# Kernel optimization log

Hardware: AMD Instinct MI355X
Metric: run time of the kernel (lower is better)

Reference implementation:

```python
import jax, jax.numpy as jnp
import numpy as np

B, C, H, W_IMG, P, D = 64, 3, 224, 224, 16, 768
N_PATCH = (H // P) * (W_IMG // P)  # 196
SEQ = N_PATCH + 1                  # 197


def setup_inputs() -> dict:
    key = jax.random.key(0)
    k1, k2, k3, k4, k5 = jax.random.split(key, 5)
    in_feat = P * P * C  # 768
    return {
        "x": jax.random.normal(k1, (B, C, H, W_IMG), dtype=jnp.float32),
        "W": jax.random.normal(k2, (in_feat, D), dtype=jnp.float32) * (1.0 / np.sqrt(in_feat)),
        "b": jax.random.normal(k3, (D,), dtype=jnp.float32) * 0.02,
        "pos_table": jax.random.normal(k4, (SEQ, D), dtype=jnp.float32) * 0.02,
        "class_token": jax.random.normal(k5, (1, 1, D), dtype=jnp.float32),
    }


def _patchify(x):
    # Matches torch loop: patch (i,j) is x[:, :, i*P:(i+1)*P, j*P:(j+1)*P].reshape(B, C*P*P)
    # i.e. features ordered channel-major then row then col within patch.
    b = x.shape[0]
    hp, wp = H // P, W_IMG // P
    x = x.reshape(b, C, hp, P, wp, P)              # (B,C,hp,P,wp,P)
    x = x.transpose(0, 2, 4, 1, 3, 5)              # (B,hp,wp,C,P,P)
    return x.reshape(b, hp * wp, C * P * P)        # (B,N,C*P*P)


def reference(x, W, b, pos_table, class_token):
    patches = _patchify(x)                          # (B, N, C*P*P)
    tokens = jnp.einsum("bnf,fd->bnd", patches, W) + b  # (B, N, D)
    cls = jnp.broadcast_to(class_token, (x.shape[0], 1, D))
    seq = jnp.concatenate([cls, tokens], axis=1)    # (B, SEQ, D)
    # positions = arange(SEQ) broadcast over batch -> embedding lookup
    return seq + pos_table[None, :, :]              # dropout is identity in eval
```

## Files before the change

### kernel.cpp

```cpp
#include <hip/hip_runtime.h>
#include <hip/hip_bf16.h>

namespace {

constexpr int Bsz = 64, Cch = 3, Himg = 224, Wimg = 224, Ppat = 16;
constexpr int Dm = 768, NPW = 14, NPATCH = 196, SEQn = 197;
constexpr int Mtot = Bsz * NPATCH;
constexpr int Ktot = 768, Ntot = 768;
constexpr int BM = 64, BN = 128, BK = 64;
constexpr int MT = Mtot / BM;
constexpr int NT = Ntot / BN;
constexpr int KT = Ktot / BK;
constexpr int NBLK = MT * NT;
constexpr int TAF = BM * BK;
constexpr int TB = BN * BK;
constexpr size_t WT_ELEMS = (size_t)NT * KT * TB;
constexpr size_t WS_NEED = WT_ELEMS * 2;
constexpr int WPREP_BLK = (Ktot / 8) * Ntot / 256;
constexpr int CLS_BLK = Bsz * Dm / 256;

typedef __attribute__((ext_vector_type(8))) short bf16x8;
typedef __attribute__((ext_vector_type(4))) float f32x4;

__device__ inline unsigned short f2bf(float f) {
  __bf16 h = (__bf16)f;
  union { __bf16 h; unsigned short u; } c;
  c.h = h;
  return c.u;
}

union Pack8 { unsigned short s[8]; uint4 v; };

__global__ void prep_kernel(const float* __restrict__ W,
                            const float* __restrict__ pos, const float* __restrict__ cls,
                            unsigned short* __restrict__ Wt, float* __restrict__ out) {
  const int bid = blockIdx.x;
  const int t = threadIdx.x;
  if (bid < WPREP_BLK) {
    int cid = bid * 256 + t;
    int kc = cid / Ntot;
    int n = cid - kc * Ntot;
    int nb = n >> 7;
    int np = n & 127;
    int kt = kc >> 3;
    int k8 = (kc & 7) * 8;
    Pack8 p;
#pragma unroll
    for (int j = 0; j < 8; ++j) p.s[j] = f2bf(W[(size_t)(kc * 8 + j) * Ntot + n]);
    int sidx = (np * BK + k8) ^ ((np & 7) << 3);
    *reinterpret_cast<uint4*>(Wt + (size_t)(nb * KT + kt) * TB + sidx) = p.v;
  } else {
    int i = (bid - WPREP_BLK) * 256 + t;
    int b = i / Dm;
    int d = i - b * Dm;
    out[(size_t)b * (SEQn * Dm) + d] = cls[d] + pos[d];
  }
}

__global__ __launch_bounds__(128, 2)
void gemm_kernel(const float* __restrict__ x, const unsigned short* __restrict__ Wt,
                 const float* __restrict__ bias, const float* __restrict__ pos,
                 float* __restrict__ out) {
  __shared__ float Af[TAF];
  __shared__ unsigned short B[TB];

  const int orig = blockIdx.x;
  const int wg = (orig & 7) * (NBLK / 8) + (orig >> 3);
  const int bm = wg / NT;
  const int bn = wg - bm * NT;

  const int t = threadIdx.x;
  const int lane = t & 63;
  const int wc = t >> 6;
  const int fr = lane & 15, fq = lane >> 4;

  const int klocal = (((t & 15) ^ ((t >> 4) & 7)) << 2);
  int rowbase[8];
#pragma unroll
  for (int i = 0; i < 8; ++i) {
    int r = i * 8 + (t >> 4);
    int m = bm * BM + r;
    int b = m / NPATCH;
    int pidx = m - b * NPATCH;
    int ph = pidx / NPW, pw = pidx - ph * NPW;
    rowbase[i] = ((b * Cch) * Himg + ph * Ppat) * Wimg + pw * Ppat;
  }
  const unsigned short* bSrc = Wt + (size_t)(bn * KT) * TB + t * 8;

  auto STAGE = [&](int kt) {
    int kg = kt * BK + klocal;
    int c = kg >> 8, pi = (kg >> 4) & 15, pj = kg & 15;
    int koff = (c * Himg + pi) * Wimg + pj;
#pragma unroll
    for (int i = 0; i < 8; ++i)
      __builtin_amdgcn_global_load_lds(
          (const __attribute__((address_space(1))) unsigned int*)(x + rowbase[i] + koff),
          (__attribute__((address_space(3))) unsigned int*)(&Af[t * 4 + i * 512]),
          16, 0, 0);
#pragma unroll
    for (int i = 0; i < 8; ++i)
      __builtin_amdgcn_global_load_lds(
          (const __attribute__((address_space(1))) unsigned int*)(bSrc + kt * TB + i * 1024),
          (__attribute__((address_space(3))) unsigned int*)(&B[t * 8 + i * 1024]),
          16, 0, 0);
  };

  f32x4 acc[4][4];
#pragma unroll
  for (int mi = 0; mi < 4; ++mi)
#pragma unroll
    for (int ni = 0; ni < 4; ++ni) acc[mi][ni] = {0.f, 0.f, 0.f, 0.f};

  for (int kt = 0; kt < KT; ++kt) {
    STAGE(kt);
    __syncthreads();
#pragma unroll
    for (int ks = 0; ks < 2; ++ks) {
      bf16x8 af[4], bfr[4];
#pragma unroll
      for (int mi = 0; mi < 4; ++mi) {
        int r = mi * 16 + fr;
        int g0 = ks * 8 + fq * 2;
        float4 a0 = *reinterpret_cast<const float4*>(&Af[r * 64 + ((g0 ^ (r & 7)) << 2)]);
        float4 a1 = *reinterpret_cast<const float4*>(&Af[r * 64 + (((g0 + 1) ^ (r & 7)) << 2)]);
        Pack8 p;
        p.s[0] = f2bf(a0.x); p.s[1] = f2bf(a0.y); p.s[2] = f2bf(a0.z); p.s[3] = f2bf(a0.w);
        p.s[4] = f2bf(a1.x); p.s[5] = f2bf(a1.y); p.s[6] = f2bf(a1.z); p.s[7] = f2bf(a1.w);
        af[mi] = *reinterpret_cast<const bf16x8*>(&p);
      }
#pragma unroll
      for (int ni = 0; ni < 4; ++ni) {
        int n = wc * 64 + ni * 16 + fr;
        int idx = (n * BK + ks * 32 + fq * 8) ^ ((n & 7) << 3);
        bfr[ni] = *reinterpret_cast<const bf16x8*>(&B[idx]);
      }
#pragma unroll
      for (int mi = 0; mi < 4; ++mi)
#pragma unroll
        for (int ni = 0; ni < 4; ++ni)
          acc[mi][ni] = __builtin_amdgcn_mfma_f32_16x16x32_bf16(
              af[mi], bfr[ni], acc[mi][ni], 0, 0, 0);
    }
    if (kt + 1 < KT) __syncthreads();
  }

  const int n0 = bn * BN + wc * 64;
  float bv[4];
#pragma unroll
  for (int ni = 0; ni < 4; ++ni) bv[ni] = bias[n0 + ni * 16 + fr];
#pragma unroll
  for (int mi = 0; mi < 4; ++mi) {
#pragma unroll
    for (int j = 0; j < 4; ++j) {
      int m = bm * BM + mi * 16 + fq * 4 + j;
      int b = m / NPATCH;
      int s = m - b * NPATCH + 1;
      float* orow = out + ((size_t)b * SEQn + s) * Dm + n0;
      const float* prow = pos + (size_t)s * Dm + n0;
#pragma unroll
      for (int ni = 0; ni < 4; ++ni) {
        int d = ni * 16 + fr;
        orow[d] = acc[mi][ni][j] + bv[ni] + prow[d];
      }
    }
  }
}

}

extern "C" void kernel_launch(void* const* d_in, const int* in_sizes, int n_in,
                              void* d_out, int out_size, void* d_ws, size_t ws_size,
                              hipStream_t stream) {
  const float* x = (const float*)d_in[0];
  const float* W = (const float*)d_in[1];
  const float* bias = (const float*)d_in[2];
  const float* pos = (const float*)d_in[3];
  const float* cls = (const float*)d_in[4];
  float* out = (float*)d_out;
  unsigned short* Wt = (unsigned short*)d_ws;

  prep_kernel<<<WPREP_BLK + CLS_BLK, 256, 0, stream>>>(W, pos, cls, Wt, out);
  gemm_kernel<<<NBLK, 128, 0, stream>>>(x, Wt, bias, pos, out);
}
```

Baseline: 46.31 us.

## Convert A tile to bf16 once at staging and use 4 waves per block

The activation tile is now loaded into registers with plain vector loads, converted to bf16 once, and written to a swizzled bf16 LDS buffer, instead of being copied as fp32 straight to LDS and reconverted by every wave on every fragment read. The block grows from 2 to 4 waves in a 2x2 layout, each holding half the accumulators, and the launch bounds ask for higher occupancy. This removes redundant conversions and halves A-tile LDS use. The cost is that the A load no longer goes asynchronously into LDS, so global latency sits in registers before the barrier.

New measurement: 38.74 us (median of 2 runs). -16.3%, faster.

```diff
diff --git a/kernel.cpp b/kernel.cpp
--- a/kernel.cpp
+++ b/kernel.cpp
@@ -12,10 +12,9 @@
 constexpr int NT = Ntot / BN;
 constexpr int KT = Ktot / BK;
 constexpr int NBLK = MT * NT;
-constexpr int TAF = BM * BK;
+constexpr int TA = BM * BK;
 constexpr int TB = BN * BK;
 constexpr size_t WT_ELEMS = (size_t)NT * KT * TB;
-constexpr size_t WS_NEED = WT_ELEMS * 2;
 constexpr int WPREP_BLK = (Ktot / 8) * Ntot / 256;
 constexpr int CLS_BLK = Bsz * Dm / 256;
 
@@ -57,11 +56,11 @@
   }
 }
 
-__global__ __launch_bounds__(128, 2)
+__global__ __launch_bounds__(256, 5)
 void gemm_kernel(const float* __restrict__ x, const unsigned short* __restrict__ Wt,
                  const float* __restrict__ bias, const float* __restrict__ pos,
                  float* __restrict__ out) {
-  __shared__ float Af[TAF];
+  __shared__ unsigned short A[TA];
   __shared__ unsigned short B[TB];
 
   const int orig = blockIdx.x;
@@ -71,62 +70,62 @@
 
   const int t = threadIdx.x;
   const int lane = t & 63;
-  const int wc = t >> 6;
+  const int wid = t >> 6;
+  const int wr = wid >> 1, wc = wid & 1;
   const int fr = lane & 15, fq = lane >> 4;
 
-  const int klocal = (((t & 15) ^ ((t >> 4) & 7)) << 2);
-  int rowbase[8];
+  const int c4 = t & 15;
+  const int r0 = t >> 4;
+  int a_base[4];
 #pragma unroll
-  for (int i = 0; i < 8; ++i) {
-    int r = i * 8 + (t >> 4);
-    int m = bm * BM + r;
+  for (int i = 0; i < 4; ++i) {
+    int m = bm * BM + r0 + 16 * i;
     int b = m / NPATCH;
     int pidx = m - b * NPATCH;
-    int ph = pidx / NPW, pw = pidx - ph * NPW;
-    rowbase[i] = ((b * Cch) * Himg + ph * Ppat) * Wimg + pw * Ppat;
+    int ph = pidx / NPW;
+    int pw = pidx - ph * NPW;
+    a_base[i] = ((b * Cch) * Himg + ph * Ppat) * Wimg + pw * Ppat;
   }
   const unsigned short* bSrc = Wt + (size_t)(bn * KT) * TB + t * 8;
 
-  auto STAGE = [&](int kt) {
-    int kg = kt * BK + klocal;
-    int c = kg >> 8, pi = (kg >> 4) & 15, pj = kg & 15;
-    int koff = (c * Himg + pi) * Wimg + pj;
+  f32x4 acc[2][4];
 #pragma unroll
-    for (int i = 0; i < 8; ++i)
-      __builtin_amdgcn_global_load_lds(
-          (const __attribute__((address_space(1))) unsigned int*)(x + rowbase[i] + koff),
-          (__attribute__((address_space(3))) unsigned int*)(&Af[t * 4 + i * 512]),
-          16, 0, 0);
-#pragma unroll
-    for (int i = 0; i < 8; ++i)
-      __builtin_amdgcn_global_load_lds(
-          (const __attribute__((address_space(1))) unsigned int*)(bSrc + kt * TB + i * 1024),
-          (__attribute__((address_space(3))) unsigned int*)(&B[t * 8 + i * 1024]),
-          16, 0, 0);
-  };
-
-  f32x4 acc[4][4];
-#pragma unroll
-  for (int mi = 0; mi < 4; ++mi)
+  for (int mi = 0; mi < 2; ++mi)
 #pragma unroll
     for (int ni = 0; ni < 4; ++ni) acc[mi][ni] = {0.f, 0.f, 0.f, 0.f};
 
   for (int kt = 0; kt < KT; ++kt) {
-    STAGE(kt);
+    float4 av[4];
+    {
+      int kg = kt * BK + c4 * 4;
+      int c = kg >> 8, pi = (kg >> 4) & 15, pj = kg & 15;
+      int off = (c * Himg + pi) * Wimg + pj;
+#pragma unroll
+      for (int i = 0; i < 4; ++i)
+        av[i] = *reinterpret_cast<const float4*>(x + a_base[i] + off);
+    }
+#pragma unroll
+    for (int i = 0; i < 4; ++i)
+      __builtin_amdgcn_global_load_lds(
+          (const __attribute__((address_space(1))) unsigned int*)(bSrc + kt * TB + i * 2048),
+          (__attribute__((address_space(3))) unsigned int*)(&B[t * 8 + i * 2048]),
+          16, 0, 0);
+#pragma unroll
+    for (int i = 0; i < 4; ++i) {
+      int row = r0 + 16 * i;
+      int idx = (row * BK + c4 * 4) ^ ((row & 7) << 3);
+      ushort4 pk = make_ushort4(f2bf(av[i].x), f2bf(av[i].y), f2bf(av[i].z), f2bf(av[i].w));
+      *reinterpret_cast<ushort4*>(&A[idx]) = pk;
+    }
     __syncthreads();
 #pragma unroll
     for (int ks = 0; ks < 2; ++ks) {
-      bf16x8 af[4], bfr[4];
+      bf16x8 af[2], bfr[4];
 #pragma unroll
-      for (int mi = 0; mi < 4; ++mi) {
-        int r = mi * 16 + fr;
-        int g0 = ks * 8 + fq * 2;
-        float4 a0 = *reinterpret_cast<const float4*>(&Af[r * 64 + ((g0 ^ (r & 7)) << 2)]);
-        float4 a1 = *reinterpret_cast<const float4*>(&Af[r * 64 + (((g0 + 1) ^ (r & 7)) << 2)]);
-        Pack8 p;
-        p.s[0] = f2bf(a0.x); p.s[1] = f2bf(a0.y); p.s[2] = f2bf(a0.z); p.s[3] = f2bf(a0.w);
-        p.s[4] = f2bf(a1.x); p.s[5] = f2bf(a1.y); p.s[6] = f2bf(a1.z); p.s[7] = f2bf(a1.w);
-        af[mi] = *reinterpret_cast<const bf16x8*>(&p);
+      for (int mi = 0; mi < 2; ++mi) {
+        int row = wr * 32 + mi * 16 + fr;
+        int idx = (row * BK + ks * 32 + fq * 8) ^ ((row & 7) << 3);
+        af[mi] = *reinterpret_cast<const bf16x8*>(&A[idx]);
       }
 #pragma unroll
       for (int ni = 0; ni < 4; ++ni) {
@@ -135,7 +134,7 @@
         bfr[ni] = *reinterpret_cast<const bf16x8*>(&B[idx]);
       }
 #pragma unroll
-      for (int mi = 0; mi < 4; ++mi)
+      for (int mi = 0; mi < 2; ++mi)
 #pragma unroll
         for (int ni = 0; ni < 4; ++ni)
           acc[mi][ni] = __builtin_amdgcn_mfma_f32_16x16x32_bf16(
@@ -149,10 +148,10 @@
 #pragma unroll
   for (int ni = 0; ni < 4; ++ni) bv[ni] = bias[n0 + ni * 16 + fr];
 #pragma unroll
-  for (int mi = 0; mi < 4; ++mi) {
+  for (int mi = 0; mi < 2; ++mi) {
 #pragma unroll
     for (int j = 0; j < 4; ++j) {
-      int m = bm * BM + mi * 16 + fq * 4 + j;
+      int m = bm * BM + wr * 32 + mi * 16 + fq * 4 + j;
       int b = m / NPATCH;
       int s = m - b * NPATCH + 1;
       float* orow = out + ((size_t)b * SEQn + s) * Dm + n0;
@@ -180,5 +179,5 @@
   unsigned short* Wt = (unsigned short*)d_ws;
 
   prep_kernel<<<WPREP_BLK + CLS_BLK, 256, 0, stream>>>(W, pos, cls, Wt, out);
-  gemm_kernel<<<NBLK, 128, 0, stream>>>(x, Wt, bias, pos, out);
+  gemm_kernel<<<NBLK, 256, 0, stream>>>(x, Wt, bias, pos, out);
 }
```
